# Kernel optimization log

Hardware: AMD Instinct MI355X
Metric: run time of the kernel (lower is better)

The kernel has to match this reference:

```python
import jax, jax.numpy as jnp
import numpy as np

IN_BIT = 8      # in_bit_width
W_BIT = 2       # weight_bit_width (also output act quantizer bit width)
BN_EPS = 1e-4


def _ste(x, q):
    # straight-through estimator: forward = q, backward = identity w.r.t. x
    return x + jax.lax.stop_gradient(q - x)


def act_quant(x, bit):
    # CommonActQuant: signed int quant, narrow_range=False, power-of-two scale
    # range [-1, 1 - 2^{-(bit-1)}] -> scale = 2^{-(bit-1)}
    s = 2.0 ** (1 - bit)
    n_min = -(2.0 ** (bit - 1))
    n_max = 2.0 ** (bit - 1) - 1.0
    q = jnp.clip(jnp.round(x / s), n_min, n_max) * s
    return _ste(x, q)


def weight_quant(w, bit):
    # CommonWeightQuant: narrow-range signed int quant, unit scaling const
    # scale = 1 / (2^{bit-1} - 1); for bit=2 levels are {-1, 0, 1}
    n = 2.0 ** (bit - 1) - 1.0
    s = 1.0 / n
    q = jnp.clip(jnp.round(w / s), -n, n) * s
    return _ste(w, q)


def setup_inputs() -> dict:
    key = jax.random.key(0)
    k1, k2, k3, k4 = jax.random.split(key, 4)
    B, C, H, W = 32, 256, 32, 32
    x = jax.random.normal(k1, (B, C, H, W), dtype=jnp.float32) * 0.5
    weight = jax.random.normal(k2, (C, C, 3, 3), dtype=jnp.float32) * 0.5
    gamma = jnp.ones((C,), dtype=jnp.float32)
    beta = jnp.zeros((C,), dtype=jnp.float32)
    running_mean = jax.random.normal(k3, (C,), dtype=jnp.float32) * 0.1
    running_var = jax.random.uniform(k4, (C,), dtype=jnp.float32, minval=0.5, maxval=1.5)
    return {"x": x, "weight": weight, "gamma": gamma, "beta": beta,
            "running_mean": running_mean, "running_var": running_var}


def reference(x, weight, gamma, beta, running_mean, running_var):
    # 1) input QuantIdentity (8-bit, [-1, 1-2^-7], power-of-two scale 2^-7)
    xq = act_quant(x, IN_BIT)
    # 2) QuantConv2d 3x3 stride 1 pad 1, no bias, 2-bit weights
    wq = weight_quant(weight, W_BIT)
    y = jax.lax.conv_general_dilated(
        xq, wq, window_strides=(1, 1), padding=((1, 1), (1, 1)),
        dimension_numbers=("NCHW", "OIHW", "NCHW"))
    # 3) BatchNorm2d (inference, eps=1e-4)
    inv = gamma / jnp.sqrt(running_var + BN_EPS)
    y = y * inv[None, :, None, None] + (beta - running_mean * inv)[None, :, None, None]
    # 4) output QuantIdentity at weight_bit_width bits
    return act_quant(y, W_BIT)
```

## Files before the change

kernel.cpp:

```cpp
#include <hip/hip_runtime.h>
#include <hip/hip_bf16.h>
#include <stdint.h>


typedef int i32x4 __attribute__((ext_vector_type(4)));
typedef float f32x4 __attribute__((ext_vector_type(4)));

__device__ __forceinline__ void gload_lds16(const void* g, const void* lds) {
    __builtin_amdgcn_global_load_lds(
        (const __attribute__((address_space(1))) unsigned int*)(uintptr_t)g,
        (__attribute__((address_space(3))) unsigned int*)(uintptr_t)lds,
        16, 0, 0);
}

__global__ __launch_bounds__(256) void quant_kernel(
    const float* __restrict__ x, const float* __restrict__ w,
    signed char* __restrict__ xpad, signed char* __restrict__ wq)
{
    __shared__ signed char tile[32 * 272];
    const int t = threadIdx.x;
    const int blk = blockIdx.x;

    if (blk >= 1088) {
        const int co = blk - 1088;
        signed char* wt = tile;
#pragma unroll
        for (int p = 0; p < 9; ++p) {
            const int idx = p * 256 + t;
            const float v = w[co * 2304 + idx];
            const int ci = idx / 9;
            const int khkw = idx - 9 * ci;
            const float q = fminf(fmaxf(rintf(v), -1.f), 1.f);
            wt[khkw * 256 + ci] = (signed char)(int)q;
        }
        __syncthreads();
        if (t < 144) {
            const int kt = t >> 2, kq = t & 3;
            const uint4 v = *(const uint4*)(wt + t * 16);
            *(uint4*)(wq + ((size_t)((co >> 4) * 36 + kt) << 10) + kq * 256 + (co & 15) * 16) = v;
        }
        return;
    }

    const int b = blk / 34;
    const int hp = blk % 34;
    signed char* rowbase = xpad + (size_t)((b * 34 + hp) * 34) * 256;
    const uint4 z = {0u, 0u, 0u, 0u};
    if (hp == 0 || hp == 33) {
        for (int i = t; i < 544; i += 256) *(uint4*)(rowbase + i * 16) = z;
        return;
    }
    const int h = hp - 1;
    const float* xb = x + ((size_t)(b * 256) * 32 + h) * 32;

#pragma unroll
    for (int q2 = 0; q2 < 2; ++q2) {
        const int beta = q2 * 256 + t;
        const int cib = beta >> 3;
        const int w4 = beta & 7;
        unsigned row[4];
#pragma unroll
        for (int j = 0; j < 4; ++j) {
            const f32x4 v = *(const f32x4*)(xb + (size_t)(cib * 4 + j) * 1024 + w4 * 4);
            unsigned p = 0;
#pragma unroll
            for (int k = 0; k < 4; ++k) {
                const float q = fminf(fmaxf(rintf(__fmul_rn(v[k], 128.f)), -128.f), 127.f);
                p |= ((unsigned)(unsigned char)(signed char)(int)q) << (8 * k);
            }
            row[j] = p;
        }
        const unsigned ab_lo = __builtin_amdgcn_perm(row[1], row[0], 0x05010400u);
        const unsigned ab_hi = __builtin_amdgcn_perm(row[1], row[0], 0x07030602u);
        const unsigned cd_lo = __builtin_amdgcn_perm(row[3], row[2], 0x05010400u);
        const unsigned cd_hi = __builtin_amdgcn_perm(row[3], row[2], 0x07030602u);
        unsigned col[4];
        col[0] = __builtin_amdgcn_perm(cd_lo, ab_lo, 0x05040100u);
        col[1] = __builtin_amdgcn_perm(cd_lo, ab_lo, 0x07060302u);
        col[2] = __builtin_amdgcn_perm(cd_hi, ab_hi, 0x05040100u);
        col[3] = __builtin_amdgcn_perm(cd_hi, ab_hi, 0x07060302u);
#pragma unroll
        for (int r = 0; r < 4; ++r)
            *(unsigned*)(tile + (w4 * 4 + r) * 272 + cib * 4) = col[r];
    }
    __syncthreads();
#pragma unroll
    for (int q = 0; q < 2; ++q) {
        const int wp = q * 16 + (t >> 4);
        const int ci16 = (t & 15) * 16;
        uint4 v = *(const uint4*)(tile + wp * 272 + ci16);
        *(uint4*)(rowbase + (size_t)(wp + 1) * 256 + ci16) = v;
    }
    if (t < 32) {
        const int wp = (t >> 4) * 33;
        *(uint4*)(rowbase + (size_t)wp * 256 + (t & 15) * 16) = z;
    }
}

__global__ __launch_bounds__(512, 4) void conv_gemm_kernel(
    const signed char* __restrict__ xpad, const signed char* __restrict__ wqm,
    const float* __restrict__ gamma, const float* __restrict__ beta,
    const float* __restrict__ mean, const float* __restrict__ var,
    float* __restrict__ out)
{
    __shared__ signed char As[6 * 34 * 256];

    const int tid = threadIdx.x;
    const int wv = tid >> 6;
    const int lane = tid & 63;
    const int l16 = lane & 15;
    const int l4 = lane >> 4;

    const int mt = blockIdx.x >> 1;
    const int n0 = (blockIdx.x & 1) * 128;
    const int b = mt >> 3;
    const int h0 = (mt & 7) * 4;
    const int wave_m = wv & 1;
    const int wave_n = wv >> 1;

    const signed char* xbase = xpad + (size_t)(b * 34 + h0) * 34 * 256;
#pragma unroll
    for (int p = 0; p < 7; ++p) {
        const int i = p * 8 + wv;
        if (i < 51) {
            const int d = i * 64 + lane;
            const int r = d >> 4;
            const int c = d & 15;
            gload_lds16(xbase + r * 256 + ((c ^ (r & 15)) << 4), As + i * 1024);
        }
    }
    __syncthreads();

    int r0[4];
#pragma unroll
    for (int i = 0; i < 4; ++i)
        r0[i] = (wave_m * 2 + (i >> 1)) * 34 + (i & 1) * 16 + l16;

    const signed char* bp0 = wqm + (((size_t)((n0 >> 4) + wave_n * 2 + 0) * 36) << 10) + lane * 16;
    const signed char* bp1 = wqm + (((size_t)((n0 >> 4) + wave_n * 2 + 1) * 36) << 10) + lane * 16;

    i32x4 acc[4][2];
#pragma unroll
    for (int i = 0; i < 4; i++)
#pragma unroll
        for (int j = 0; j < 2; j++) acc[i][j] = (i32x4){0, 0, 0, 0};

    i32x4 aP[2][4], bP[2][2];

#define LOAD_B(kt, dst) { dst[0] = *(const i32x4*)(bp0 + (kt) * 1024); \
                          dst[1] = *(const i32x4*)(bp1 + (kt) * 1024); }
#define LOAD_A(kt, dst) { const int khkw = (kt) >> 2; \
                          const int kh = khkw / 3; \
                          const int kw = khkw - 3 * kh; \
                          const int roff = kh * 34 + kw; \
                          const int cb = ((kt) & 3) * 4 + l4; \
                          _Pragma("unroll") \
                          for (int i = 0; i < 4; ++i) { \
                              const int r = r0[i] + roff; \
                              dst[i] = *(const i32x4*)(As + r * 256 + ((cb ^ (r & 15)) << 4)); \
                          } }
#define MFMA(af, bf) { _Pragma("unroll") \
                       for (int i = 0; i < 4; ++i) \
                           _Pragma("unroll") \
                           for (int j = 0; j < 2; ++j) \
                               acc[i][j] = __builtin_amdgcn_mfma_i32_16x16x64_i8(af[i], bf[j], acc[i][j], 0, 0, 0); }

    LOAD_B(0, bP[0])
    LOAD_A(0, aP[0])
#pragma unroll
    for (int kt = 0; kt < 36; ++kt) {
        const int cur = kt & 1, nxt = cur ^ 1;
        if (kt + 1 < 36) { LOAD_B(kt + 1, bP[nxt]) LOAD_A(kt + 1, aP[nxt]) }
        MFMA(aP[cur], bP[cur])
    }

#pragma unroll
    for (int j = 0; j < 2; ++j) {
        const int co = n0 + wave_n * 32 + j * 16 + l16;
        const float iv = __fdiv_rn(gamma[co], __fsqrt_rn(__fadd_rn(var[co], 1e-4f)));
        const float bias = __fsub_rn(beta[co], __fmul_rn(mean[co], iv));
#pragma unroll
        for (int i = 0; i < 4; ++i) {
            const int h = h0 + wave_m * 2 + (i >> 1);
            const int w = (i & 1) * 16 + l4 * 4;
            f32x4 v;
#pragma unroll
            for (int r = 0; r < 4; r++) {
                const float y = __fmul_rn((float)acc[i][j][r], 0.0078125f);
                const float t = __fadd_rn(__fmul_rn(y, iv), bias);
                float z = rintf(__fmul_rn(t, 2.f));
                z = fminf(fmaxf(z, -2.f), 1.f);
                v[r] = __fmul_rn(z, 0.5f);
            }
            *(f32x4*)(&out[(((size_t)(b * 256 + co)) * 32 + h) * 32 + w]) = v;
        }
    }
#undef LOAD_B
#undef LOAD_A
#undef MFMA
}

extern "C" void kernel_launch(void* const* d_in, const int* in_sizes, int n_in,
                              void* d_out, int out_size, void* d_ws, size_t ws_size,
                              hipStream_t stream) {
    const float* x      = (const float*)d_in[0];
    const float* weight = (const float*)d_in[1];
    const float* gamma  = (const float*)d_in[2];
    const float* beta   = (const float*)d_in[3];
    const float* rmean  = (const float*)d_in[4];
    const float* rvar   = (const float*)d_in[5];
    float* out = (float*)d_out;

    signed char* wq   = (signed char*)d_ws;
    signed char* xpad = (signed char*)d_ws + (1 << 20);

    quant_kernel<<<1344, 256, 0, stream>>>(x, weight, xpad, wq);
    conv_gemm_kernel<<<512, 512, 0, stream>>>(xpad, wq, gamma, beta, rmean, rvar, out);
}
```

Before: 115.7 us.

## Enlarge conv tile to 8 output rows and split the input-halo LDS load

After: 127.2 us. 1.1x slower.

```diff
diff --git a/kernel.cpp b/kernel.cpp
--- a/kernel.cpp
+++ b/kernel.cpp
@@ -97,13 +97,13 @@
     }
 }
 
-__global__ __launch_bounds__(512, 4) void conv_gemm_kernel(
+__global__ __launch_bounds__(512, 2) void conv_gemm_kernel(
     const signed char* __restrict__ xpad, const signed char* __restrict__ wqm,
     const float* __restrict__ gamma, const float* __restrict__ beta,
     const float* __restrict__ mean, const float* __restrict__ var,
     float* __restrict__ out)
 {
-    __shared__ signed char As[6 * 34 * 256];
+    __shared__ signed char As[10 * 34 * 256];
 
     const int tid = threadIdx.x;
     const int wv = tid >> 6;
@@ -113,16 +113,14 @@
 
     const int mt = blockIdx.x >> 1;
     const int n0 = (blockIdx.x & 1) * 128;
-    const int b = mt >> 3;
-    const int h0 = (mt & 7) * 4;
-    const int wave_m = wv & 1;
-    const int wave_n = wv >> 1;
+    const int b = mt >> 2;
+    const int h0 = (mt & 3) * 8;
 
     const signed char* xbase = xpad + (size_t)(b * 34 + h0) * 34 * 256;
 #pragma unroll
-    for (int p = 0; p < 7; ++p) {
+    for (int p = 0; p < 9; ++p) {
         const int i = p * 8 + wv;
-        if (i < 51) {
+        if (i < 68) {
             const int d = i * 64 + lane;
             const int r = d >> 4;
             const int c = d & 15;
@@ -130,59 +128,83 @@
         }
     }
     __syncthreads();
-
-    int r0[4];
-#pragma unroll
-    for (int i = 0; i < 4; ++i)
-        r0[i] = (wave_m * 2 + (i >> 1)) * 34 + (i & 1) * 16 + l16;
-
-    const signed char* bp0 = wqm + (((size_t)((n0 >> 4) + wave_n * 2 + 0) * 36) << 10) + lane * 16;
-    const signed char* bp1 = wqm + (((size_t)((n0 >> 4) + wave_n * 2 + 1) * 36) << 10) + lane * 16;
-
-    i32x4 acc[4][2];
-#pragma unroll
-    for (int i = 0; i < 4; i++)
-#pragma unroll
-        for (int j = 0; j < 2; j++) acc[i][j] = (i32x4){0, 0, 0, 0};
-
-    i32x4 aP[2][4], bP[2][2];
-
-#define LOAD_B(kt, dst) { dst[0] = *(const i32x4*)(bp0 + (kt) * 1024); \
-                          dst[1] = *(const i32x4*)(bp1 + (kt) * 1024); }
+#pragma unroll
+    for (int p = 0; p < 3; ++p) {
+        const int i = 68 + p * 8 + wv;
+        if (i < 85) {
+            const int d = i * 64 + lane;
+            const int r = d >> 4;
+            const int c = d & 15;
+            gload_lds16(xbase + r * 256 + ((c ^ (r & 15)) << 4), As + i * 1024);
+        }
+    }
+
+    int r0[2];
+#pragma unroll
+    for (int i = 0; i < 2; ++i)
+        r0[i] = wv * 34 + i * 16 + l16;
+
+    const signed char* bp[8];
+#pragma unroll
+    for (int j = 0; j < 8; ++j)
+        bp[j] = wqm + (((size_t)((n0 >> 4) + j) * 36) << 10) + lane * 16;
+
+    i32x4 acc[2][8];
+#pragma unroll
+    for (int i = 0; i < 2; i++)
+#pragma unroll
+        for (int j = 0; j < 8; j++) acc[i][j] = (i32x4){0, 0, 0, 0};
+
+    i32x4 aP[2][2], bP[2][8];
+
+#define LOAD_B(kt, dst) { _Pragma("unroll") \
+                          for (int j = 0; j < 8; ++j) \
+                              dst[j] = *(const i32x4*)(bp[j] + (kt) * 1024); }
 #define LOAD_A(kt, dst) { const int khkw = (kt) >> 2; \
                           const int kh = khkw / 3; \
                           const int kw = khkw - 3 * kh; \
                           const int roff = kh * 34 + kw; \
                           const int cb = ((kt) & 3) * 4 + l4; \
                           _Pragma("unroll") \
-                          for (int i = 0; i < 4; ++i) { \
+                          for (int i = 0; i < 2; ++i) { \
                               const int r = r0[i] + roff; \
                               dst[i] = *(const i32x4*)(As + r * 256 + ((cb ^ (r & 15)) << 4)); \
                           } }
 #define MFMA(af, bf) { _Pragma("unroll") \
-                       for (int i = 0; i < 4; ++i) \
+                       for (int i = 0; i < 2; ++i) \
                            _Pragma("unroll") \
-                           for (int j = 0; j < 2; ++j) \
+                           for (int j = 0; j < 8; ++j) \
                                acc[i][j] = __builtin_amdgcn_mfma_i32_16x16x64_i8(af[i], bf[j], acc[i][j], 0, 0, 0); }
 
     LOAD_B(0, bP[0])
     LOAD_A(0, aP[0])
 #pragma unroll
-    for (int kt = 0; kt < 36; ++kt) {
+    for (int kt = 0; kt < 11; ++kt) {
+        const int cur = kt & 1, nxt = cur ^ 1;
+        LOAD_B(kt + 1, bP[nxt])
+        LOAD_A(kt + 1, aP[nxt])
+        MFMA(aP[cur], bP[cur])
+    }
+    LOAD_B(12, bP[0])
+    MFMA(aP[1], bP[1])
+    __syncthreads();
+    LOAD_A(12, aP[0])
+#pragma unroll
+    for (int kt = 12; kt < 36; ++kt) {
         const int cur = kt & 1, nxt = cur ^ 1;
         if (kt + 1 < 36) { LOAD_B(kt + 1, bP[nxt]) LOAD_A(kt + 1, aP[nxt]) }
         MFMA(aP[cur], bP[cur])
     }
 
-#pragma unroll
-    for (int j = 0; j < 2; ++j) {
-        const int co = n0 + wave_n * 32 + j * 16 + l16;
+    const int h = h0 + wv;
+#pragma unroll
+    for (int j = 0; j < 8; ++j) {
+        const int co = n0 + j * 16 + l16;
         const float iv = __fdiv_rn(gamma[co], __fsqrt_rn(__fadd_rn(var[co], 1e-4f)));
         const float bias = __fsub_rn(beta[co], __fmul_rn(mean[co], iv));
 #pragma unroll
-        for (int i = 0; i < 4; ++i) {
-            const int h = h0 + wave_m * 2 + (i >> 1);
-            const int w = (i & 1) * 16 + l4 * 4;
+        for (int i = 0; i < 2; ++i) {
+            const int w = i * 16 + l4 * 4;
             f32x4 v;
 #pragma unroll
             for (int r = 0; r < 4; r++) {
@@ -215,5 +237,5 @@
     signed char* xpad = (signed char*)d_ws + (1 << 20);
 
     quant_kernel<<<1344, 256, 0, stream>>>(x, weight, xpad, wq);
-    conv_gemm_kernel<<<512, 512, 0, stream>>>(xpad, wq, gamma, beta, rmean, rvar, out);
-}
+    conv_gemm_kernel<<<256, 512, 0, stream>>>(xpad, wq, gamma, beta, rmean, rvar, out);
+}
```
